# Optimization experiments

Hardware: AMD Instinct MI355X
Metric: run time of the kernel (lower is better)

## Reference

```python
import jax, jax.numpy as jnp
import numpy as np

# Dimensions (match init_kwargs / input_specs)
NF, NLOC, NALL = 1, 1024, 2048
N_DIM, E_DIM, A_DIM = 128, 16, 64
NNEI, A_SEL, AXIS = 120, 20, 4

act = jax.nn.silu


def _lin(key, i, o):
    k1, k2 = jax.random.split(key)
    w = jax.random.normal(k1, (i, o), jnp.float32) / np.float32(np.sqrt(i))
    b = jax.random.normal(k2, (o,), jnp.float32) * 0.01
    return w, b


def setup_inputs() -> dict:
    key = jax.random.key(0)
    ks = jax.random.split(key, 16)
    d = {}
    d["node_ebd_ext"] = jax.random.normal(ks[0], (NF, NALL, N_DIM), jnp.float32)
    d["edge_ebd"] = jax.random.normal(ks[1], (NF, NLOC, NNEI, E_DIM), jnp.float32)
    d["h2"] = jax.random.normal(ks[2], (NF, NLOC, NNEI, 3), jnp.float32)
    d["angle_ebd"] = jax.random.normal(ks[3], (NF, NLOC, A_SEL, A_SEL, A_DIM), jnp.float32)
    d["sw"] = jax.random.uniform(ks[4], (NF, NLOC, NNEI), jnp.float32)
    d["a_sw"] = jax.random.uniform(ks[5], (NF, NLOC, A_SEL), jnp.float32)
    d["nlist"] = jax.random.randint(ks[6], (NF, NLOC, NNEI), 0, NALL)
    d["nlist_mask"] = jnp.ones((NF, NLOC, NNEI), bool)
    d["a_nlist_mask"] = jnp.ones((NF, NLOC, A_SEL), bool)
    edge_info_dim = 2 * N_DIM + E_DIM          # 272
    angle_dim = A_DIM + N_DIM + 2 * E_DIM      # 224 (a_compress_rate == 0)
    d["w_node_self"], d["b_node_self"] = _lin(ks[7], N_DIM, N_DIM)
    d["w_node_sym"], d["b_node_sym"] = _lin(ks[8], (N_DIM + E_DIM) * AXIS, N_DIM)
    d["w_node_edge"], d["b_node_edge"] = _lin(ks[9], edge_info_dim, N_DIM)
    d["w_edge_self"], d["b_edge_self"] = _lin(ks[10], edge_info_dim, E_DIM)
    d["w_ea1"], d["b_ea1"] = _lin(ks[11], angle_dim, E_DIM)
    d["w_ea2"], d["b_ea2"] = _lin(ks[12], E_DIM, E_DIM)
    d["w_angle_self"], d["b_angle_self"] = _lin(ks[13], angle_dim, A_DIM)
    # res_residual update style: one learnable residual scale per update branch,
    # init 'const' with update_residual = 0.1
    d["n_res"] = jnp.full((3, N_DIM), 0.1, jnp.float32)  # self, sym, edge-message
    d["e_res"] = jnp.full((2, E_DIM), 0.1, jnp.float32)  # self, angle-message
    d["a_res"] = jnp.full((1, A_DIM), 0.1, jnp.float32)  # self
    return d


def _forward(node_ebd_ext, edge_ebd, h2, angle_ebd, sw, a_sw,
             w_node_self, b_node_self, w_node_sym, b_node_sym,
             w_node_edge, b_node_edge, w_edge_self, b_edge_self,
             w_ea1, b_ea1, w_ea2, b_ea2, w_angle_self, b_angle_self,
             n_res, e_res, a_res, nlist, nlist_mask, a_nlist_mask):
    nf, nall, n_dim = node_ebd_ext.shape
    _, nloc, nnei, e_dim = edge_ebd.shape
    a_sel = angle_ebd.shape[2]
    node_ebd = node_ebd_ext[:, :nloc]

    # gather neighbor node embeddings: nf x nloc x nnei x n_dim
    nei_node = jax.vmap(lambda tbl, idx: tbl[idx])(node_ebd_ext, nlist)
    nei_node = jnp.where(nlist_mask[..., None], nei_node, 0.0)

    # 1) node self update
    node_self_update = act(node_ebd @ w_node_self + b_node_self)

    # 2) node symmetrization update (grrg over both edge and neighbor-node features)
    wgt = (sw * nlist_mask)[..., None]

    def sym(ebd):
        e = ebd * wgt
        hg = jnp.einsum('flni,flnd->flid', h2, e) / np.float32(nnei)  # f,l,3,d
        grrg = jnp.einsum('flid,flia->flda', hg, hg[..., :AXIS]) / np.float32(3.0)
        return grrg.reshape(nf, nloc, -1)

    node_sym_in = jnp.concatenate([sym(nei_node), sym(edge_ebd)], axis=-1)
    node_sym_update = act(node_sym_in @ w_node_sym + b_node_sym)

    # 3) edge info = [node_i, node_j, edge_ij]
    node_i = jnp.broadcast_to(node_ebd[:, :, None, :], (nf, nloc, nnei, n_dim))
    edge_info = jnp.concatenate([node_i, nei_node, edge_ebd], axis=-1)

    # 3a) node <- edge message (sw-weighted mean over neighbors)
    node_edge_update = act(edge_info @ w_node_edge + b_node_edge) * sw[..., None]
    node_edge_update = node_edge_update.sum(axis=-2) / np.float32(nnei)

    node_new = (node_ebd + n_res[0] * node_self_update
                + n_res[1] * node_sym_update + n_res[2] * node_edge_update)

    # 4) edge self update
    edge_self_update = act(edge_info @ w_edge_self + b_edge_self)

    # 5) angle branch (a_compress_rate == 0)
    edge_for_angle = jnp.where(a_nlist_mask[..., None], edge_ebd[:, :, :a_sel, :], 0.0)
    node_angle = jnp.broadcast_to(node_ebd[:, :, None, None, :], (nf, nloc, a_sel, a_sel, n_dim))
    e_ik = jnp.broadcast_to(edge_for_angle[:, :, :, None, :], (nf, nloc, a_sel, a_sel, e_dim))
    e_ij = jnp.broadcast_to(edge_for_angle[:, :, None, :, :], (nf, nloc, a_sel, a_sel, e_dim))
    angle_info = jnp.concatenate([angle_ebd, node_angle, e_ik, e_ij], axis=-1)

    # edge <- angle message: sw-weighted reduce over one angle axis
    ea = act(angle_info @ w_ea1 + b_ea1)  # nf,nloc,a_sel,a_sel,e_dim
    weighted = a_sw[:, :, :, None, None] * a_sw[:, :, None, :, None] * ea
    reduced = weighted.sum(axis=-2) / np.float32(np.sqrt(a_sel))  # nf,nloc,a_sel,e_dim
    pad = jnp.zeros((nf, nloc, nnei - a_sel, e_dim), edge_ebd.dtype)
    padded = jnp.concatenate([reduced, pad], axis=2)
    full_mask = jnp.concatenate(
        [a_nlist_mask, jnp.zeros((nf, nloc, nnei - a_sel), bool)], axis=-1)
    # smooth_edge_update = False: keep original edge ebd where angle mask is off
    padded = jnp.where(full_mask[..., None], padded, edge_ebd)
    edge_angle_update = act(padded @ w_ea2 + b_ea2)

    edge_new = edge_ebd + e_res[0] * edge_self_update + e_res[1] * edge_angle_update

    # angle self update
    angle_self_update = act(angle_info @ w_angle_self + b_angle_self)
    angle_new = angle_ebd + a_res[0] * angle_self_update

    return node_new, edge_new, angle_new


def reference(node_ebd_ext, edge_ebd, h2, angle_ebd, sw, a_sw, nlist, nlist_mask,
              a_nlist_mask, w_node_self, b_node_self, w_node_sym, b_node_sym,
              w_node_edge, b_node_edge, w_edge_self, b_edge_self, w_ea1, b_ea1,
              w_ea2, b_ea2, w_angle_self, b_angle_self, n_res, e_res, a_res):
    return _forward(node_ebd_ext, edge_ebd, h2, angle_ebd, sw, a_sw,
                    w_node_self, b_node_self, w_node_sym, b_node_sym,
                    w_node_edge, b_node_edge, w_edge_self, b_edge_self,
                    w_ea1, b_ea1, w_ea2, b_ea2, w_angle_self, b_angle_self,
                    n_res, e_res, a_res, nlist, nlist_mask, a_nlist_mask)
```

## Files before the change

### kernel.cpp

```cpp
#include <hip/hip_runtime.h>
#include <math.h>

#define NLOC 1024
#define NALL 2048
#define NDIM 128
#define EDIM 16
#define ADIM 64
#define NNEI 120
#define ASEL 20


__device__ __forceinline__ float silu(float x) {
    return x * __builtin_amdgcn_rcpf(1.f + __expf(-x));
}

__device__ __forceinline__ unsigned short f2bf(float f) {
    unsigned int u = __float_as_uint(f);
    u += 0x7fffu + ((u >> 16) & 1u);
    return (unsigned short)(u >> 16);
}

typedef __attribute__((ext_vector_type(8))) short bf16x8;
typedef __attribute__((ext_vector_type(4))) float f32x4;

__global__ __launch_bounds__(256) void k_prep(
    const float* __restrict__ node_ext,
    const float* __restrict__ w_ne, const float* __restrict__ b_ne,
    const float* __restrict__ w_es, const float* __restrict__ b_es,
    const float* __restrict__ w_ea1, const float* __restrict__ b_ea1,
    const float* __restrict__ w_as, const float* __restrict__ b_as,
    float* __restrict__ proj, float* __restrict__ pre_e,
    float* __restrict__ pre_a, unsigned short* __restrict__ wtb)
{
    const int b = blockIdx.x, t = threadIdx.x;
    if (b == 3072) {
        for (int idx = t; idx < 64 * 80; idx += 256) {
            int k = idx / 80, o = idx - k * 80;
            float v = (o < 16) ? w_ea1[k * 16 + o] : w_as[k * 64 + (o - 16)];
            wtb[o * 64 + k] = f2bf(v);
        }
        return;
    }
    __shared__ float x[128];
    const int row = (b < 2048) ? b : (b - 2048);
    if (t < 128) x[t] = node_ext[row * 128 + t];
    __syncthreads();
    if (b < 2048) {
        if (t < 144) {
            float acc = 0.f;
            if (t < 128) {
                for (int k = 0; k < 128; k++) acc += x[k] * w_ne[(128 + k) * 128 + t];
            } else {
                int o = t - 128;
                for (int k = 0; k < 128; k++) acc += x[k] * w_es[(128 + k) * 16 + o];
            }
            proj[b * 144 + t] = acc;
        }
    } else {
        int i = b - 2048;
        if (t < 144) {
            float acc;
            if (t < 128) {
                acc = b_ne[t];
                for (int k = 0; k < 128; k++) acc += x[k] * w_ne[k * 128 + t];
            } else {
                int o = t - 128;
                acc = b_es[o];
                for (int k = 0; k < 128; k++) acc += x[k] * w_es[k * 16 + o];
            }
            pre_e[i * 144 + t] = acc;
        } else if (t < 224) {
            int o = t - 144;
            float acc;
            if (o < 16) {
                acc = b_ea1[o];
                for (int k = 0; k < 128; k++) acc += x[k] * w_ea1[(64 + k) * 16 + o];
            } else {
                int o2 = o - 16;
                acc = b_as[o2];
                for (int k = 0; k < 128; k++) acc += x[k] * w_as[(64 + k) * 64 + o2];
            }
            pre_a[i * 80 + o] = acc;
        }
    }
}

__global__ __launch_bounds__(256, 4) void k_angle(
    const float* __restrict__ angle, const float* __restrict__ edge,
    const float* __restrict__ asw,
    const float* __restrict__ w_ea1, const float* __restrict__ w_as,
    const unsigned short* __restrict__ wtb, const float* __restrict__ pre_a,
    const float* __restrict__ a_res,
    float* __restrict__ out_angle, float* __restrict__ reduced)
{
    const int i = blockIdx.x >> 1, h = blockIdx.x & 1, t = threadIdx.x;
    const int lane = t & 63, wv = t >> 6;
    const int m = lane & 15, q = lane >> 4;
    const int mt_lo = h ? 15 : 0, mt_hi = h ? 25 : 15;

    __shared__ float eca_s[ASEL * 80], ecb_s[ASEL * 80], edge20_s[ASEL * EDIM];
    __shared__ float asw_s[ASEL], ares_s[ADIM], red_s[ASEL * 16];

    bf16x8 bfrag[5][2];
    #pragma unroll
    for (int nt = 0; nt < 5; nt++)
        #pragma unroll
        for (int ks = 0; ks < 2; ks++)
            bfrag[nt][ks] = *(const bf16x8*)&wtb[(nt * 16 + m) * 64 + ks * 32 + q * 8];

    for (int idx = t; idx < ASEL * EDIM; idx += 256)
        edge20_s[idx] = edge[(size_t)i * NNEI * EDIM + idx];
    if (t < ASEL) asw_s[t] = asw[i * ASEL + t];
    if (t < ADIM) ares_s[t] = a_res[t];
    for (int idx = t; idx < ASEL * 16; idx += 256) red_s[idx] = 0.f;
    __syncthreads();

    int mt = mt_lo + wv;
    float4 c0, c1, c2, c3;
    {
        const float* Arow = angle + ((size_t)i * 400 + mt * 16 + m) * 64 + q * 8;
        c0 = *(const float4*)(Arow + 0);
        c1 = *(const float4*)(Arow + 4);
        c2 = *(const float4*)(Arow + 32);
        c3 = *(const float4*)(Arow + 36);
    }

    for (int idx = t; idx < 2 * ASEL * 80; idx += 256) {
        int half = idx / 1600, rem = idx - half * 1600;
        int aa = rem / 80, o = rem - aa * 80;
        float acc = (half == 0) ? pre_a[i * 80 + o] : 0.f;
        if (o < 16) {
            const float* w = w_ea1 + (192 + half * 16) * 16 + o;
            #pragma unroll
            for (int k = 0; k < 16; k++) acc += edge20_s[aa * 16 + k] * w[k * 16];
        } else {
            const float* w = w_as + (192 + half * 16) * 64 + (o - 16);
            #pragma unroll
            for (int k = 0; k < 16; k++) acc += edge20_s[aa * 16 + k] * w[k * 64];
        }
        if (half == 0) eca_s[rem] = acc; else ecb_s[rem] = acc;
    }
    __syncthreads();

    for (; mt < mt_hi; mt += 4) {
        const int nmt = mt + 4;
        float4 n0{}, n1{}, n2{}, n3{};
        if (nmt < mt_hi) {
            const float* Arow = angle + ((size_t)i * 400 + nmt * 16 + m) * 64 + q * 8;
            n0 = *(const float4*)(Arow + 0);
            n1 = *(const float4*)(Arow + 4);
            n2 = *(const float4*)(Arow + 32);
            n3 = *(const float4*)(Arow + 36);
        }

        bf16x8 af0, af1;
        af0[0] = (short)f2bf(c0.x); af0[1] = (short)f2bf(c0.y);
        af0[2] = (short)f2bf(c0.z); af0[3] = (short)f2bf(c0.w);
        af0[4] = (short)f2bf(c1.x); af0[5] = (short)f2bf(c1.y);
        af0[6] = (short)f2bf(c1.z); af0[7] = (short)f2bf(c1.w);
        af1[0] = (short)f2bf(c2.x); af1[1] = (short)f2bf(c2.y);
        af1[2] = (short)f2bf(c2.z); af1[3] = (short)f2bf(c2.w);
        af1[4] = (short)f2bf(c3.x); af1[5] = (short)f2bf(c3.y);
        af1[6] = (short)f2bf(c3.z); af1[7] = (short)f2bf(c3.w);

        const int p0 = mt * 16 + q * 4;
        float rez[4][4];
        #pragma unroll
        for (int r = 0; r < 4; r++) {
            const float* ar = angle + ((size_t)i * 400 + p0 + r) * 64 + m - 16;
            #pragma unroll
            for (int nt = 1; nt < 5; nt++) rez[r][nt - 1] = ar[nt * 16];
        }

        f32x4 acc[5];
        #pragma unroll
        for (int nt = 0; nt < 5; nt++) {
            acc[nt] = (f32x4){0.f, 0.f, 0.f, 0.f};
            acc[nt] = __builtin_amdgcn_mfma_f32_16x16x32_bf16(af0, bfrag[nt][0], acc[nt], 0, 0, 0);
            acc[nt] = __builtin_amdgcn_mfma_f32_16x16x32_bf16(af1, bfrag[nt][1], acc[nt], 0, 0, 0);
        }

        #pragma unroll
        for (int r = 0; r < 4; r++) {
            const int p = p0 + r;
            const int a = p / 20;
            const int bb = p - a * 20;
            {
                const float s = acc[0][r] + eca_s[a * 80 + m] + ecb_s[bb * 80 + m];
                atomicAdd(&red_s[a * 16 + m], asw_s[bb] * silu(s));
            }
            const size_t base = ((size_t)i * 400 + p) * 64;
            #pragma unroll
            for (int nt = 1; nt < 5; nt++) {
                const int o = nt * 16 + m;
                const float s = acc[nt][r] + eca_s[a * 80 + o] + ecb_s[bb * 80 + o];
                out_angle[base + o - 16] = rez[r][nt - 1] + ares_s[o - 16] * silu(s);
            }
        }

        c0 = n0; c1 = n1; c2 = n2; c3 = n3;
    }
    __syncthreads();

    const int lo = h ? 192 : 0, hi = h ? 320 : 192;
    for (int idx = lo + t; idx < hi; idx += 256) {
        const int aa = idx >> 4;
        reduced[i * 320 + idx] = red_s[idx] * asw_s[aa] * 0.22360679774997896f;
    }
}

__global__ __launch_bounds__(256) void k_edge(
    const float* __restrict__ edge, const float* __restrict__ sw,
    const int* __restrict__ nlist,
    const float* __restrict__ w_ne, const float* __restrict__ w_es,
    const float* __restrict__ w_ea2, const float* __restrict__ b_ea2,
    const float* __restrict__ e_res,
    const float* __restrict__ proj, const float* __restrict__ pre_e,
    const float* __restrict__ reduced,
    float* __restrict__ neu, float* __restrict__ out_edge)
{
    const int i = blockIdx.x, t = threadIdx.x;
    __shared__ float red_s[320], esu_s[120 * 17], pre_e_s[144];
    __shared__ float wea2_s[256], bea2_s[16], eres_s[32], sw_s[120];
    __shared__ float wes_s[256];
    __shared__ float edge_s[120 * 17];
    __shared__ float neu_part[2][128];
    __shared__ int nl_s[120];

    for (int idx = t; idx < 320; idx += 256) red_s[idx] = reduced[i * 320 + idx];
    for (int idx = t; idx < 1920; idx += 256) {
        const int j = idx >> 4, k = idx & 15;
        edge_s[j * 17 + k] = edge[(size_t)i * 1920 + idx];
    }
    if (t < 144) pre_e_s[t] = pre_e[i * 144 + t];
    if (t < 120) { nl_s[t] = nlist[i * 120 + t]; sw_s[t] = sw[i * 120 + t]; }
    if (t < 256) wea2_s[t] = w_ea2[t];
    if (t < 16) bea2_s[t] = b_ea2[t];
    if (t < 32) eres_s[t] = e_res[t];
    for (int idx = t; idx < 256; idx += 256) wes_s[idx] = w_es[256 * 16 + idx];
    __syncthreads();

    {
        const int o = t & 127, half = t >> 7;
        const int j0 = half * 60, j1 = j0 + 60;
        float w3c[16];
        #pragma unroll
        for (int k = 0; k < 16; k++) w3c[k] = w_ne[(256 + k) * 128 + o];
        const float pe = pre_e_s[o];
        float pj = proj[(size_t)nl_s[j0] * 144 + o];
        float acc = 0.f;
        for (int j = j0; j < j1; j++) {
            float pn = 0.f;
            if (j + 1 < j1) pn = proj[(size_t)nl_s[j + 1] * 144 + o];
            const float* er = &edge_s[j * 17];
            float s = pe + pj;
            #pragma unroll
            for (int k = 0; k < 16; k++) s += er[k] * w3c[k];
            acc += silu(s) * sw_s[j];
            pj = pn;
        }
        neu_part[half][o] = acc;
    }

    for (int idx = t; idx < 1920; idx += 256) {
        const int j = idx >> 4, oo = idx & 15;
        const int n = nl_s[j];
        float s = pre_e_s[128 + oo] + proj[(size_t)n * 144 + 128 + oo];
        #pragma unroll
        for (int k = 0; k < 16; k++) s += edge_s[j * 17 + k] * wes_s[k * 16 + oo];
        esu_s[j * 17 + oo] = silu(s);
    }
    __syncthreads();

    if (t < 128) neu[i * 128 + t] = (neu_part[0][t] + neu_part[1][t]) * (1.f / 120.f);

    for (int idx = t; idx < 1920; idx += 256) {
        const int j = idx >> 4, o = idx & 15;
        float s = bea2_s[o];
        if (j < 20) {
            #pragma unroll
            for (int k = 0; k < 16; k++) s += red_s[j * 16 + k] * wea2_s[k * 16 + o];
        } else {
            const float* er = &edge_s[j * 17];
            #pragma unroll
            for (int k = 0; k < 16; k++) s += er[k] * wea2_s[k * 16 + o];
        }
        const float eau = silu(s);
        const float ev = edge_s[j * 17 + o];
        out_edge[((size_t)i * 120 + j) * 16 + o] =
            ev + eres_s[o] * esu_s[j * 17 + o] + eres_s[16 + o] * eau;
    }
}

__global__ __launch_bounds__(256) void k_node(
    const float* __restrict__ node_ext, const float* __restrict__ edge,
    const float* __restrict__ h2, const float* __restrict__ sw,
    const int* __restrict__ nlist,
    const float* __restrict__ w_ns, const float* __restrict__ b_ns,
    const float* __restrict__ w_sym, const float* __restrict__ b_sym,
    const float* __restrict__ n_res, const float* __restrict__ neu,
    float* __restrict__ out_node)
{
    const int i = blockIdx.x, t = threadIdx.x;
    __shared__ float node_s[128], hjc_s[120 * 4], hgN_s[3 * 128], hgE_s[3 * 16], sym_s[576];
    __shared__ float hgN_part[2][3][128];
    __shared__ float hgE_part[8][3][16];
    __shared__ float s2_part[128];
    __shared__ int nl_s[120];

    if (t < 128) node_s[t] = node_ext[i * 128 + t];
    if (t < 120) {
        nl_s[t] = nlist[i * 120 + t];
        const float s = sw[i * 120 + t];
        hjc_s[t * 4 + 0] = h2[((size_t)i * 120 + t) * 3 + 0] * s;
        hjc_s[t * 4 + 1] = h2[((size_t)i * 120 + t) * 3 + 1] * s;
        hjc_s[t * 4 + 2] = h2[((size_t)i * 120 + t) * 3 + 2] * s;
        hjc_s[t * 4 + 3] = 0.f;
    }
    __syncthreads();

    {
        const int d = t & 127, half = t >> 7;
        const int j0 = half * 60, j1 = j0 + 60;
        float a0 = 0.f, a1 = 0.f, a2 = 0.f;
        float v = node_ext[(size_t)nl_s[j0] * 128 + d];
        for (int j = j0; j < j1; j++) {
            float vn = 0.f;
            if (j + 1 < j1) vn = node_ext[(size_t)nl_s[j + 1] * 128 + d];
            const float4 hc = *(const float4*)&hjc_s[j * 4];
            a0 += hc.x * v; a1 += hc.y * v; a2 += hc.z * v;
            v = vn;
        }
        hgN_part[half][0][d] = a0;
        hgN_part[half][1][d] = a1;
        hgN_part[half][2][d] = a2;
    }

    if (t < 128) {
        const int d = t & 15, ch = t >> 4;
        const int j0 = ch * 15;
        float a0 = 0.f, a1 = 0.f, a2 = 0.f;
        for (int j = j0; j < j0 + 15; j++) {
            const float v = edge[((size_t)i * 120 + j) * 16 + d];
            const float4 hc = *(const float4*)&hjc_s[j * 4];
            a0 += hc.x * v; a1 += hc.y * v; a2 += hc.z * v;
        }
        hgE_part[ch][0][d] = a0;
        hgE_part[ch][1][d] = a1;
        hgE_part[ch][2][d] = a2;
    }
    __syncthreads();

    if (t < 128) {
        hgN_s[0 * 128 + t] = (hgN_part[0][0][t] + hgN_part[1][0][t]) * (1.f / 120.f);
        hgN_s[1 * 128 + t] = (hgN_part[0][1][t] + hgN_part[1][1][t]) * (1.f / 120.f);
        hgN_s[2 * 128 + t] = (hgN_part[0][2][t] + hgN_part[1][2][t]) * (1.f / 120.f);
    } else if (t < 176) {
        const int c = (t - 128) >> 4, d = (t - 128) & 15;
        float s = 0.f;
        #pragma unroll
        for (int ch = 0; ch < 8; ch++) s += hgE_part[ch][c][d];
        hgE_s[c * 16 + d] = s * (1.f / 120.f);
    }
    __syncthreads();

    for (int idx = t; idx < 576; idx += 256) {
        if (idx < 512) {
            const int d = idx >> 2, a = idx & 3;
            sym_s[idx] = (hgN_s[d] * hgN_s[a] + hgN_s[128 + d] * hgN_s[128 + a] +
                          hgN_s[256 + d] * hgN_s[256 + a]) * (1.f / 3.f);
        } else {
            const int r = idx - 512, d = r >> 2, a = r & 3;
            sym_s[idx] = (hgE_s[d] * hgE_s[a] + hgE_s[16 + d] * hgE_s[16 + a] +
                          hgE_s[32 + d] * hgE_s[32 + a]) * (1.f / 3.f);
        }
    }
    __syncthreads();

    float s1 = 0.f, s2 = 0.f;
    {
        const int o = t & 127, half = t >> 7;
        if (half == 0) {
            s1 = b_ns[o];
            for (int k = 0; k < 128; k++) s1 += node_s[k] * w_ns[k * 128 + o];
            s2 = b_sym[o];
            for (int k = 0; k < 224; k++) s2 += sym_s[k] * w_sym[k * 128 + o];
        } else {
            for (int k = 224; k < 576; k++) s2 += sym_s[k] * w_sym[k * 128 + o];
            s2_part[o] = s2;
        }
    }
    __syncthreads();

    if (t < 128) {
        const float nsu = silu(s1);
        const float nsy = silu(s2 + s2_part[t]);
        out_node[i * 128 + t] = node_s[t] + n_res[t] * nsu + n_res[128 + t] * nsy +
                                n_res[256 + t] * neu[i * 128 + t];
    }
}

extern "C" void kernel_launch(void* const* d_in, const int* in_sizes, int n_in,
                              void* d_out, int out_size, void* d_ws, size_t ws_size,
                              hipStream_t stream)
{
    const float* node_ext = (const float*)d_in[0];
    const float* edge     = (const float*)d_in[1];
    const float* h2       = (const float*)d_in[2];
    const float* angle    = (const float*)d_in[3];
    const float* sw       = (const float*)d_in[4];
    const float* asw      = (const float*)d_in[5];
    const int*   nlist    = (const int*)d_in[6];
    const float* w_ns  = (const float*)d_in[9];  const float* b_ns  = (const float*)d_in[10];
    const float* w_sym = (const float*)d_in[11]; const float* b_sym = (const float*)d_in[12];
    const float* w_ne  = (const float*)d_in[13]; const float* b_ne  = (const float*)d_in[14];
    const float* w_es  = (const float*)d_in[15]; const float* b_es  = (const float*)d_in[16];
    const float* w_ea1 = (const float*)d_in[17]; const float* b_ea1 = (const float*)d_in[18];
    const float* w_ea2 = (const float*)d_in[19]; const float* b_ea2 = (const float*)d_in[20];
    const float* w_as  = (const float*)d_in[21]; const float* b_as  = (const float*)d_in[22];
    const float* n_res = (const float*)d_in[23];
    const float* e_res = (const float*)d_in[24];
    const float* a_res = (const float*)d_in[25];

    float* out_node  = (float*)d_out;
    float* out_edge  = out_node + (size_t)NLOC * NDIM;
    float* out_angle = out_edge + (size_t)NLOC * NNEI * EDIM;

    float* ws      = (float*)d_ws;
    float* proj    = ws;
    float* pre_e   = proj + 2048 * 144;
    float* pre_a   = pre_e + 1024 * 144;
    float* reduced = pre_a + 1024 * 80;
    float* neu     = reduced + 1024 * 320;
    unsigned short* wtb = (unsigned short*)(neu + 1024 * 128);

    k_prep<<<dim3(3073), dim3(256), 0, stream>>>(node_ext, w_ne, b_ne, w_es, b_es,
                                                 w_ea1, b_ea1, w_as, b_as,
                                                 proj, pre_e, pre_a, wtb);
    k_angle<<<dim3(2048), dim3(256), 0, stream>>>(angle, edge, asw, w_ea1, w_as,
                                                  wtb, pre_a, a_res, out_angle, reduced);
    k_edge<<<dim3(1024), dim3(256), 0, stream>>>(edge, sw, nlist, w_ne, w_es,
                                                 w_ea2, b_ea2, e_res, proj, pre_e,
                                                 reduced, neu, out_edge);
    k_node<<<dim3(1024), dim3(256), 0, stream>>>(node_ext, edge, h2, sw, nlist,
                                                 w_ns, b_ns, w_sym, b_sym, n_res,
                                                 neu, out_node);
}
```

Measured before the change: 377.9 us.

## Fuse edge and node kernels and use one angle block per atom

Merges k_edge and k_node into a single k_en kernel, so the neighbour-edge message stays in shared memory instead of going through a global buffer. The node sym step now reads edge rows from the shared tile rather than from global memory, and one launch is removed. Separately, k_angle goes from two blocks per atom to one block covering all 25 row tiles, which halves the grid and removes the duplicated per-block edge-combination setup but lowers parallelism. The fused kernel uses much more shared memory per block, which may reduce occupancy.

```diff
diff --git a/kernel.cpp b/kernel.cpp
--- a/kernel.cpp
+++ b/kernel.cpp
@@ -93,10 +93,9 @@
     const float* __restrict__ a_res,
     float* __restrict__ out_angle, float* __restrict__ reduced)
 {
-    const int i = blockIdx.x >> 1, h = blockIdx.x & 1, t = threadIdx.x;
+    const int i = blockIdx.x, t = threadIdx.x;
     const int lane = t & 63, wv = t >> 6;
     const int m = lane & 15, q = lane >> 4;
-    const int mt_lo = h ? 15 : 0, mt_hi = h ? 25 : 15;
 
     __shared__ float eca_s[ASEL * 80], ecb_s[ASEL * 80], edge20_s[ASEL * EDIM];
     __shared__ float asw_s[ASEL], ares_s[ADIM], red_s[ASEL * 16];
@@ -115,7 +114,7 @@
     for (int idx = t; idx < ASEL * 16; idx += 256) red_s[idx] = 0.f;
     __syncthreads();
 
-    int mt = mt_lo + wv;
+    int mt = wv;
     float4 c0, c1, c2, c3;
     {
         const float* Arow = angle + ((size_t)i * 400 + mt * 16 + m) * 64 + q * 8;
@@ -142,10 +141,10 @@
     }
     __syncthreads();
 
-    for (; mt < mt_hi; mt += 4) {
+    for (; mt < 25; mt += 4) {
         const int nmt = mt + 4;
         float4 n0{}, n1{}, n2{}, n3{};
-        if (nmt < mt_hi) {
+        if (nmt < 25) {
             const float* Arow = angle + ((size_t)i * 400 + nmt * 16 + m) * 64 + q * 8;
             n0 = *(const float4*)(Arow + 0);
             n1 = *(const float4*)(Arow + 4);
@@ -202,30 +201,37 @@
     }
     __syncthreads();
 
-    const int lo = h ? 192 : 0, hi = h ? 320 : 192;
-    for (int idx = lo + t; idx < hi; idx += 256) {
+    for (int idx = t; idx < ASEL * 16; idx += 256) {
         const int aa = idx >> 4;
         reduced[i * 320 + idx] = red_s[idx] * asw_s[aa] * 0.22360679774997896f;
     }
 }
 
-__global__ __launch_bounds__(256) void k_edge(
-    const float* __restrict__ edge, const float* __restrict__ sw,
-    const int* __restrict__ nlist,
+__global__ __launch_bounds__(256) void k_en(
+    const float* __restrict__ edge, const float* __restrict__ h2,
+    const float* __restrict__ sw, const int* __restrict__ nlist,
+    const float* __restrict__ node_ext,
     const float* __restrict__ w_ne, const float* __restrict__ w_es,
     const float* __restrict__ w_ea2, const float* __restrict__ b_ea2,
     const float* __restrict__ e_res,
     const float* __restrict__ proj, const float* __restrict__ pre_e,
     const float* __restrict__ reduced,
-    float* __restrict__ neu, float* __restrict__ out_edge)
+    const float* __restrict__ w_ns, const float* __restrict__ b_ns,
+    const float* __restrict__ w_sym, const float* __restrict__ b_sym,
+    const float* __restrict__ n_res,
+    float* __restrict__ out_edge, float* __restrict__ out_node)
 {
     const int i = blockIdx.x, t = threadIdx.x;
     __shared__ float red_s[320], esu_s[120 * 17], pre_e_s[144];
     __shared__ float wea2_s[256], bea2_s[16], eres_s[32], sw_s[120];
     __shared__ float wes_s[256];
     __shared__ float edge_s[120 * 17];
-    __shared__ float neu_part[2][128];
+    __shared__ float neu_part[2][128], neu_s[128];
     __shared__ int nl_s[120];
+    __shared__ float node_s[128], hjc_s[120 * 4], hgN_s[3 * 128], hgE_s[3 * 16], sym_s[576];
+    __shared__ float hgN_part[2][3][128];
+    __shared__ float hgE_part[8][3][16];
+    __shared__ float s2_part[128];
 
     for (int idx = t; idx < 320; idx += 256) red_s[idx] = reduced[i * 320 + idx];
     for (int idx = t; idx < 1920; idx += 256) {
@@ -233,7 +239,16 @@
         edge_s[j * 17 + k] = edge[(size_t)i * 1920 + idx];
     }
     if (t < 144) pre_e_s[t] = pre_e[i * 144 + t];
-    if (t < 120) { nl_s[t] = nlist[i * 120 + t]; sw_s[t] = sw[i * 120 + t]; }
+    if (t < 128) node_s[t] = node_ext[i * 128 + t];
+    if (t < 120) {
+        nl_s[t] = nlist[i * 120 + t];
+        const float s = sw[i * 120 + t];
+        sw_s[t] = s;
+        hjc_s[t * 4 + 0] = h2[((size_t)i * 120 + t) * 3 + 0] * s;
+        hjc_s[t * 4 + 1] = h2[((size_t)i * 120 + t) * 3 + 1] * s;
+        hjc_s[t * 4 + 2] = h2[((size_t)i * 120 + t) * 3 + 2] * s;
+        hjc_s[t * 4 + 3] = 0.f;
+    }
     if (t < 256) wea2_s[t] = w_ea2[t];
     if (t < 16) bea2_s[t] = b_ea2[t];
     if (t < 32) eres_s[t] = e_res[t];
@@ -272,52 +287,7 @@
     }
     __syncthreads();
 
-    if (t < 128) neu[i * 128 + t] = (neu_part[0][t] + neu_part[1][t]) * (1.f / 120.f);
-
-    for (int idx = t; idx < 1920; idx += 256) {
-        const int j = idx >> 4, o = idx & 15;
-        float s = bea2_s[o];
-        if (j < 20) {
-            #pragma unroll
-            for (int k = 0; k < 16; k++) s += red_s[j * 16 + k] * wea2_s[k * 16 + o];
-        } else {
-            const float* er = &edge_s[j * 17];
-            #pragma unroll
-            for (int k = 0; k < 16; k++) s += er[k] * wea2_s[k * 16 + o];
-        }
-        const float eau = silu(s);
-        const float ev = edge_s[j * 17 + o];
-        out_edge[((size_t)i * 120 + j) * 16 + o] =
-            ev + eres_s[o] * esu_s[j * 17 + o] + eres_s[16 + o] * eau;
-    }
-}
-
-__global__ __launch_bounds__(256) void k_node(
-    const float* __restrict__ node_ext, const float* __restrict__ edge,
-    const float* __restrict__ h2, const float* __restrict__ sw,
-    const int* __restrict__ nlist,
-    const float* __restrict__ w_ns, const float* __restrict__ b_ns,
-    const float* __restrict__ w_sym, const float* __restrict__ b_sym,
-    const float* __restrict__ n_res, const float* __restrict__ neu,
-    float* __restrict__ out_node)
-{
-    const int i = blockIdx.x, t = threadIdx.x;
-    __shared__ float node_s[128], hjc_s[120 * 4], hgN_s[3 * 128], hgE_s[3 * 16], sym_s[576];
-    __shared__ float hgN_part[2][3][128];
-    __shared__ float hgE_part[8][3][16];
-    __shared__ float s2_part[128];
-    __shared__ int nl_s[120];
-
-    if (t < 128) node_s[t] = node_ext[i * 128 + t];
-    if (t < 120) {
-        nl_s[t] = nlist[i * 120 + t];
-        const float s = sw[i * 120 + t];
-        hjc_s[t * 4 + 0] = h2[((size_t)i * 120 + t) * 3 + 0] * s;
-        hjc_s[t * 4 + 1] = h2[((size_t)i * 120 + t) * 3 + 1] * s;
-        hjc_s[t * 4 + 2] = h2[((size_t)i * 120 + t) * 3 + 2] * s;
-        hjc_s[t * 4 + 3] = 0.f;
-    }
-    __syncthreads();
+    if (t < 128) neu_s[t] = (neu_part[0][t] + neu_part[1][t]) * (1.f / 120.f);
 
     {
         const int d = t & 127, half = t >> 7;
@@ -341,13 +311,30 @@
         const int j0 = ch * 15;
         float a0 = 0.f, a1 = 0.f, a2 = 0.f;
         for (int j = j0; j < j0 + 15; j++) {
-            const float v = edge[((size_t)i * 120 + j) * 16 + d];
+            const float v = edge_s[j * 17 + d];
             const float4 hc = *(const float4*)&hjc_s[j * 4];
             a0 += hc.x * v; a1 += hc.y * v; a2 += hc.z * v;
         }
         hgE_part[ch][0][d] = a0;
         hgE_part[ch][1][d] = a1;
         hgE_part[ch][2][d] = a2;
+    }
+
+    for (int idx = t; idx < 1920; idx += 256) {
+        const int j = idx >> 4, o = idx & 15;
+        float s = bea2_s[o];
+        if (j < 20) {
+            #pragma unroll
+            for (int k = 0; k < 16; k++) s += red_s[j * 16 + k] * wea2_s[k * 16 + o];
+        } else {
+            const float* er = &edge_s[j * 17];
+            #pragma unroll
+            for (int k = 0; k < 16; k++) s += er[k] * wea2_s[k * 16 + o];
+        }
+        const float eau = silu(s);
+        const float ev = edge_s[j * 17 + o];
+        out_edge[((size_t)i * 120 + j) * 16 + o] =
+            ev + eres_s[o] * esu_s[j * 17 + o] + eres_s[16 + o] * eau;
     }
     __syncthreads();
 
@@ -396,7 +383,7 @@
         const float nsu = silu(s1);
         const float nsy = silu(s2 + s2_part[t]);
         out_node[i * 128 + t] = node_s[t] + n_res[t] * nsu + n_res[128 + t] * nsy +
-                                n_res[256 + t] * neu[i * 128 + t];
+                                n_res[256 + t] * neu_s[t];
     }
 }
 
@@ -431,18 +418,16 @@
     float* pre_e   = proj + 2048 * 144;
     float* pre_a   = pre_e + 1024 * 144;
     float* reduced = pre_a + 1024 * 80;
-    float* neu     = reduced + 1024 * 320;
-    unsigned short* wtb = (unsigned short*)(neu + 1024 * 128);
+    unsigned short* wtb = (unsigned short*)(reduced + 1024 * 320);
 
     k_prep<<<dim3(3073), dim3(256), 0, stream>>>(node_ext, w_ne, b_ne, w_es, b_es,
                                                  w_ea1, b_ea1, w_as, b_as,
                                                  proj, pre_e, pre_a, wtb);
-    k_angle<<<dim3(2048), dim3(256), 0, stream>>>(angle, edge, asw, w_ea1, w_as,
+    k_angle<<<dim3(1024), dim3(256), 0, stream>>>(angle, edge, asw, w_ea1, w_as,
                                                   wtb, pre_a, a_res, out_angle, reduced);
-    k_edge<<<dim3(1024), dim3(256), 0, stream>>>(edge, sw, nlist, w_ne, w_es,
-                                                 w_ea2, b_ea2, e_res, proj, pre_e,
-                                                 reduced, neu, out_edge);
-    k_node<<<dim3(1024), dim3(256), 0, stream>>>(node_ext, edge, h2, sw, nlist,
-                                                 w_ns, b_ns, w_sym, b_sym, n_res,
-                                                 neu, out_node);
-}
+    k_en<<<dim3(1024), dim3(256), 0, stream>>>(edge, h2, sw, nlist, node_ext,
+                                               w_ne, w_es, w_ea2, b_ea2, e_res,
+                                               proj, pre_e, reduced,
+                                               w_ns, b_ns, w_sym, b_sym, n_res,
+                                               out_edge, out_node);
+}
```

After: 351.9 us. 1.07x faster.
